# Kernel tuning notes

Measured on AMD Instinct MI355X. Metric: run time of the kernel, lower is better.

## Reference

```python
import jax, jax.numpy as jnp
import numpy as np

KS = 4          # kernel_size per pseudo-dim (open linear B-splines, degree 1)
GRID = 28       # level-0 grid side
BATCH = 256     # number of graphs
NUM_FIRST_FC = 49


def _grid(n, B):
    """Batched 8-neighborhood grid graph with 2D pseudo-coords in [0,1]."""
    rs, cs = np.meshgrid(np.arange(n), np.arange(n), indexing='ij')
    idx = rs * n + cs
    src_l, dst_l, ps_l = [], [], []
    for dr in (-1, 0, 1):
        for dc in (-1, 0, 1):
            if dr == 0 and dc == 0:
                continue
            r2, c2 = rs + dr, cs + dc
            ok = (r2 >= 0) & (r2 < n) & (c2 >= 0) & (c2 < n)
            src_l.append(idx[ok])
            dst_l.append((r2 * n + c2)[ok])
            m = int(ok.sum())
            ps_l.append(np.stack([np.full(m, (dr + 1) / 2.0),
                                  np.full(m, (dc + 1) / 2.0)], 1))
    src = np.concatenate(src_l)
    dst = np.concatenate(dst_l)
    pseudo = np.concatenate(ps_l).astype(np.float32)
    off = (np.arange(B) * n * n)[:, None]
    src_b = (src[None] + off).reshape(-1)
    dst_b = (dst[None] + off).reshape(-1)
    return (np.stack([src_b, dst_b]).astype(np.int32),
            np.tile(pseudo, (B, 1)))


def _cluster(n, B):
    """Factor-4 (2x2 block) graclus-style cluster assignment, batched."""
    rs, cs = np.meshgrid(np.arange(n), np.arange(n), indexing='ij')
    c = ((rs // 2) * (n // 2) + (cs // 2)).reshape(-1)
    off = (np.arange(B) * (n // 2) ** 2)[:, None]
    return (c[None] + off).reshape(-1).astype(np.int32)


def setup_inputs() -> dict:
    key = jax.random.key(0)
    ks = jax.random.split(key, 16)
    e0, p0 = _grid(GRID, BATCH)          # 28x28 level
    e1, p1 = _grid(GRID // 2, BATCH)     # 14x14 level
    c0 = _cluster(GRID, BATCH)           # 784 -> 196 per graph
    c1 = _cluster(GRID // 2, BATCH)      # 196 -> 49 per graph
    N0 = BATCH * GRID * GRID
    s = 0.1
    inp = {
        'x': jax.random.normal(ks[0], (N0, 1), jnp.float32),
        'edge_index0': jnp.asarray(e0), 'pseudo0': jnp.asarray(p0),
        'edge_index1': jnp.asarray(e1), 'pseudo1': jnp.asarray(p1),
        'cluster0': jnp.asarray(c0), 'cluster1': jnp.asarray(c1),
        'W1': s * jax.random.normal(ks[1], (16, 1, 32), jnp.float32),
        'root1': s * jax.random.normal(ks[2], (1, 32), jnp.float32),
        'b1': jnp.zeros((32,), jnp.float32),
        'W2': s * jax.random.normal(ks[3], (16, 32, 32), jnp.float32),
        'root2': s * jax.random.normal(ks[4], (32, 32), jnp.float32),
        'b2': jnp.zeros((32,), jnp.float32),
        'W3': s * jax.random.normal(ks[5], (16, 32, 64), jnp.float32),
        'root3': s * jax.random.normal(ks[6], (32, 64), jnp.float32),
        'b3': jnp.zeros((64,), jnp.float32),
        'W4': s * jax.random.normal(ks[7], (16, 64, 64), jnp.float32),
        'root4': s * jax.random.normal(ks[8], (64, 64), jnp.float32),
        'b4': jnp.zeros((64,), jnp.float32),
        'fc1_W': s * jax.random.normal(ks[9], (NUM_FIRST_FC * 64, 512), jnp.float32),
        'fc1_b': jnp.zeros((512,), jnp.float32),
        'fc2_W': s * jax.random.normal(ks[10], (512, 10), jnp.float32),
        'fc2_b': jnp.zeros((10,), jnp.float32),
    }
    return inp


def spline_conv(x, src, dst, pseudo, W, root, bias):
    """SplineGCN layer: degree-1 open B-spline weighting over 2D pseudo-coords,
    mean aggregation over incoming edges, plus root weight and bias."""
    n = x.shape[0]
    pos = pseudo * (KS - 1)                       # [E,2] in [0, KS-1]
    i0f = jnp.clip(jnp.floor(pos), 0, KS - 2)
    frac = pos - i0f                              # [E,2]
    i0 = i0f.astype(jnp.int32)
    XW = jnp.einsum('ni,kio->kno', x, W)          # [K, N, out]: per-kernel transform
    msg = jnp.zeros((src.shape[0], W.shape[2]), x.dtype)
    for a in (0, 1):
        wa = frac[:, 0] if a else 1.0 - frac[:, 0]
        for b in (0, 1):
            wb = frac[:, 1] if b else 1.0 - frac[:, 1]
            k = (i0[:, 0] + a) * KS + (i0[:, 1] + b)     # flat kernel index [E]
            msg = msg + (wa * wb)[:, None] * XW[k, src]  # gather per-edge
    agg = jax.ops.segment_sum(msg, dst, num_segments=n)
    deg = jax.ops.segment_sum(jnp.ones_like(dst, dtype=x.dtype), dst,
                              num_segments=n)
    return agg / jnp.maximum(deg, 1.0)[:, None] + x @ root + bias


def pool4(x, cluster):
    # GraclusMaxPool(2): two halving levels == factor-4 cluster max-pool
    return jax.ops.segment_max(x, cluster, num_segments=x.shape[0] // 4)


def reference(x, edge_index0, pseudo0, edge_index1, pseudo1, cluster0, cluster1,
              W1, root1, b1, W2, root2, b2, W3, root3, b3, W4, root4, b4,
              fc1_W, fc1_b, fc2_W, fc2_b):
    s0, d0 = edge_index0[0], edge_index0[1]
    s1, d1 = edge_index1[0], edge_index1[1]
    h = jax.nn.elu(spline_conv(x, s0, d0, pseudo0, W1, root1, b1))
    h = jax.nn.elu(spline_conv(h, s0, d0, pseudo0, W2, root2, b2))
    h = pool4(h, cluster0)
    h = jax.nn.elu(spline_conv(h, s1, d1, pseudo1, W3, root3, b3))
    h = jax.nn.elu(spline_conv(h, s1, d1, pseudo1, W4, root4, b4))
    h = pool4(h, cluster1)
    h = h.reshape(-1, NUM_FIRST_FC * 64)           # [B, 49*64]
    h = jax.nn.elu(h @ fc1_W + fc1_b)
    # dropout is identity in eval / deterministic reference
    logits = h @ fc2_W + fc2_b
    return jax.nn.log_softmax(logits, axis=-1)
```

## Files before the change

kernel.cpp:

```cpp
#include <hip/hip_runtime.h>

typedef unsigned short u16;
typedef short bf16x8 __attribute__((ext_vector_type(8)));
typedef float f32x4 __attribute__((ext_vector_type(4)));

__device__ __constant__ const int DRS[8] = {-1,-1,-1, 0, 0, 1, 1, 1};
__device__ __constant__ const int DCS[8] = {-1, 0, 1,-1, 1,-1, 0, 1};

__device__ inline float bf2f(u16 u) { return __uint_as_float(((unsigned)u) << 16); }
__device__ inline u16 f2bf(float f) {
  unsigned u = __float_as_uint(f);
  return (u16)((u + 0x7fffu + ((u >> 16) & 1u)) >> 16);
}
__device__ inline float eluf(float v) { return v > 0.f ? v : (__expf(v) - 1.f); }

__device__ inline float weff_val(const float* __restrict__ W, int d, int off, int stride) {
  int dd = d >= 4 ? d + 1 : d;
  int dr = dd / 3 - 1, dc = dd - (dd / 3) * 3 - 1;
  int kr0, kr1, nr; float wr0, wr1;
  if (dr < 0)       { kr0 = 0; wr0 = 1.f; kr1 = 0; wr1 = 0.f; nr = 1; }
  else if (dr == 0) { kr0 = 1; wr0 = .5f; kr1 = 2; wr1 = .5f; nr = 2; }
  else              { kr0 = 3; wr0 = 1.f; kr1 = 0; wr1 = 0.f; nr = 1; }
  int kc0, kc1, nc; float wc0, wc1;
  if (dc < 0)       { kc0 = 0; wc0 = 1.f; kc1 = 0; wc1 = 0.f; nc = 1; }
  else if (dc == 0) { kc0 = 1; wc0 = .5f; kc1 = 2; wc1 = .5f; nc = 2; }
  else              { kc0 = 3; wc0 = 1.f; kc1 = 0; wc1 = 0.f; nc = 1; }
  float acc = wr0 * wc0 * W[(kr0 * 4 + kc0) * stride + off];
  if (nc == 2) acc += wr0 * wc1 * W[(kr0 * 4 + kc1) * stride + off];
  if (nr == 2) {
    acc += wr1 * wc0 * W[(kr1 * 4 + kc0) * stride + off];
    if (nc == 2) acc += wr1 * wc1 * W[(kr1 * 4 + kc1) * stride + off];
  }
  return acc;
}

__global__ __launch_bounds__(256) void pack_all(
    const float* __restrict__ W1,
    const float* __restrict__ W2, const float* __restrict__ rt2,
    const float* __restrict__ W3, const float* __restrict__ rt3,
    const float* __restrict__ W4, const float* __restrict__ rt4,
    const float* __restrict__ fcW,
    float* __restrict__ wf1, u16* __restrict__ wp2,
    u16* __restrict__ wp3, u16* __restrict__ wp4, u16* __restrict__ wfc) {
  int idx = blockIdx.x * 256 + threadIdx.x;
  if (idx < 256) {
    int d = idx >> 5, o = idx & 31;
    wf1[idx] = weff_val(W1, d, o, 32);
    return;
  }
  if (idx < 9472) {
    int local = idx - 256;
    int j = local & 7, l = (local >> 3) & 63, chunk = local >> 9;
    int ct = chunk & 1, tap = chunk >> 1;
    int k = (l >> 4) * 8 + j, n = ct * 16 + (l & 15);
    float v = tap < 8 ? weff_val(W2, tap, k * 32 + n, 1024) : rt2[k * 32 + n];
    wp2[local] = f2bf(v);
    return;
  }
  if (idx < 27904) {
    int local = idx - 9472;
    int j = local & 7, l = (local >> 3) & 63, chunk = local >> 9;
    int ct = chunk & 3, tap = chunk >> 2;
    int k = (l >> 4) * 8 + j, n = ct * 16 + (l & 15);
    float v = tap < 8 ? weff_val(W3, tap, k * 64 + n, 2048) : rt3[k * 64 + n];
    wp3[local] = f2bf(v);
    return;
  }
  if (idx < 64768) {
    int local = idx - 27904;
    int j = local & 7, l = (local >> 3) & 63, chunk = local >> 9;
    int q = chunk & 1, tmp = chunk >> 1;
    int ct = tmp & 3, tap = tmp >> 2;
    int k = q * 32 + (l >> 4) * 8 + j, n = ct * 16 + (l & 15);
    float v = tap < 8 ? weff_val(W4, tap, k * 64 + n, 4096) : rt4[k * 64 + n];
    wp4[local] = f2bf(v);
    return;
  }
  {
    int local = idx - 64768;
    int j = local & 7, l = (local >> 3) & 63, qnt = local >> 9;
    int q = qnt >> 5, nt = qnt & 31;
    int k = q * 32 + (l >> 4) * 8 + j;
    int n = nt * 16 + (l & 15);
    wfc[local] = f2bf(fcW[(size_t)k * 512 + n]);
  }
}

__global__ __launch_bounds__(512) void conv_mega(
    const float* __restrict__ x,
    const float* __restrict__ wf1, const float* __restrict__ rt1, const float* __restrict__ b1,
    const u16* __restrict__ wp2, const float* __restrict__ b2,
    const u16* __restrict__ wp3, const float* __restrict__ b3,
    const u16* __restrict__ wp4, const float* __restrict__ b4,
    u16* __restrict__ A6) {
  extern __shared__ char smem[];
  int4* H1 = (int4*)smem;
  int4* H3 = (int4*)smem;
  u16*  H5 = (u16*)(smem + 17408);
  float* XT = (float*)(smem + 61568);
  int4* H2 = (int4*)(smem + 61568);
  u16*  H2u = (u16*)(smem + 61568);
  int4* H4 = (int4*)(smem + 61568);
  u16*  H4u = (u16*)(smem + 61568);

  int img = blockIdx.x, tid = threadIdx.x;
  int lane = tid & 63, wid = tid >> 6;
  int kcb = lane >> 4, n0 = lane & 15;
  int4 z4 = make_int4(0, 0, 0, 0);

  bf16x8 w2[9][2];
#pragma unroll
  for (int tap = 0; tap < 9; ++tap)
#pragma unroll
    for (int cc = 0; cc < 2; ++cc)
      w2[tap][cc] = *(const bf16x8*)(wp2 + (tap * 2 + cc) * 512 + lane * 8);

  for (int i = tid; i < 3848; i += 512) H1[i] = z4;
  for (int i = tid; i < 960; i += 512) XT[i] = 0.f;
  __syncthreads();
  for (int i = tid; i < 784; i += 512) {
    int r = i / 28, c = i - 28 * (i / 28);
    XT[(r + 1) * 32 + c + 1] = x[(size_t)img * 784 + i];
  }
  __syncthreads();

  for (int px = tid; px < 784; px += 512) {
    int r = px / 28, c = px - 28 * (px / 28);
    float acc[32];
#pragma unroll
    for (int o = 0; o < 32; ++o) acc[o] = 0.f;
#pragma unroll
    for (int d = 0; d < 8; ++d) {
      float xv = XT[(r + 1 - DRS[d]) * 32 + (c + 1 - DCS[d])];
#pragma unroll
      for (int o = 0; o < 32; ++o) acc[o] = fmaf(xv, wf1[d * 32 + o], acc[o]);
    }
    float inv = 1.f / (float)((3 - (r == 0) - (r == 27)) * (3 - (c == 0) - (c == 27)) - 1);
    float xc = XT[(r + 1) * 32 + c + 1];
    unsigned pk[16];
#pragma unroll
    for (int h = 0; h < 16; ++h) {
      float v0 = eluf(acc[2 * h] * inv + xc * rt1[2 * h] + b1[2 * h]);
      float v1 = eluf(acc[2 * h + 1] * inv + xc * rt1[2 * h + 1] + b1[2 * h + 1]);
      pk[h] = (unsigned)f2bf(v0) | ((unsigned)f2bf(v1) << 16);
    }
#pragma unroll
    for (int kc = 0; kc < 4; ++kc)
      H1[kc * 962 + (r + 1) * 32 + (c + 1)] =
          make_int4(pk[4 * kc], pk[4 * kc + 1], pk[4 * kc + 2], pk[4 * kc + 3]);
  }
  __syncthreads();

  for (int t = wid; t < 49; t += 8) {
    int pxm = t * 16 + n0;
    int r = pxm / 28, c = pxm - 28 * (pxm / 28);
    f32x4 an0 = {0,0,0,0}, an1 = {0,0,0,0}, ar0 = {0,0,0,0}, ar1 = {0,0,0,0};
#pragma unroll
    for (int d = 0; d < 8; ++d) {
      bf16x8 a = *(const bf16x8*)&H1[kcb * 962 + (r + 1 - DRS[d]) * 32 + (c + 1 - DCS[d])];
      an0 = __builtin_amdgcn_mfma_f32_16x16x32_bf16(a, w2[d][0], an0, 0, 0, 0);
      an1 = __builtin_amdgcn_mfma_f32_16x16x32_bf16(a, w2[d][1], an1, 0, 0, 0);
    }
    {
      bf16x8 a = *(const bf16x8*)&H1[kcb * 962 + (r + 1) * 32 + (c + 1)];
      ar0 = __builtin_amdgcn_mfma_f32_16x16x32_bf16(a, w2[8][0], ar0, 0, 0, 0);
      ar1 = __builtin_amdgcn_mfma_f32_16x16x32_bf16(a, w2[8][1], ar1, 0, 0, 0);
    }
#pragma unroll
    for (int j = 0; j < 4; ++j) {
      int pm = t * 16 + (lane >> 4) * 4 + j;
      int rm = pm / 28, cm = pm - 28 * (pm / 28);
      float inv = 1.f / (float)((3 - (rm == 0) - (rm == 27)) * (3 - (cm == 0) - (cm == 27)) - 1);
      H2u[pm * 32 + n0]      = f2bf(eluf(an0[j] * inv + ar0[j] + b2[n0]));
      H2u[pm * 32 + 16 + n0] = f2bf(eluf(an1[j] * inv + ar1[j] + b2[16 + n0]));
    }
  }
  __syncthreads();

  for (int i = tid; i < 1032; i += 512) {
    int kc = i / 258, rem = i - 258 * kc;
    int4 v = z4;
    if (rem < 256) {
      int pr = rem >> 4, pc = rem & 15;
      if (pr >= 1 && pr <= 14 && pc >= 1 && pc <= 14) {
        int px0 = (2 * (pr - 1)) * 28 + 2 * (pc - 1);
        union { int4 q; u16 s[8]; } A, B, C, D, R;
        A.q = H2[px0 * 4 + kc]; B.q = H2[(px0 + 1) * 4 + kc];
        C.q = H2[(px0 + 28) * 4 + kc]; D.q = H2[(px0 + 29) * 4 + kc];
#pragma unroll
        for (int e = 0; e < 8; ++e)
          R.s[e] = f2bf(fmaxf(fmaxf(bf2f(A.s[e]), bf2f(B.s[e])),
                              fmaxf(bf2f(C.s[e]), bf2f(D.s[e]))));
        v = R.q;
      }
    }
    H3[i] = v;
  }
  __syncthreads();

  int ctg = wid & 3, t0 = wid >> 2;
  bf16x8 w3[9];
#pragma unroll
  for (int tap = 0; tap < 9; ++tap)
    w3[tap] = *(const bf16x8*)(wp3 + (tap * 4 + ctg) * 512 + lane * 8);
  for (int i = tid; i < 2064; i += 512) H4[i] = z4;
  __syncthreads();

  for (int t = t0; t < 13; t += 2) {
    int pxm = t * 16 + n0; if (pxm > 195) pxm = 195;
    int r = pxm / 14, c = pxm - 14 * (pxm / 14);
    f32x4 an = {0,0,0,0}, ar = {0,0,0,0};
#pragma unroll
    for (int d = 0; d < 8; ++d) {
      bf16x8 a = *(const bf16x8*)&H3[kcb * 258 + (r + 1 - DRS[d]) * 16 + (c + 1 - DCS[d])];
      an = __builtin_amdgcn_mfma_f32_16x16x32_bf16(a, w3[d], an, 0, 0, 0);
    }
    {
      bf16x8 a = *(const bf16x8*)&H3[kcb * 258 + (r + 1) * 16 + (c + 1)];
      ar = __builtin_amdgcn_mfma_f32_16x16x32_bf16(a, w3[8], ar, 0, 0, 0);
    }
#pragma unroll
    for (int j = 0; j < 4; ++j) {
      int pm = t * 16 + (lane >> 4) * 4 + j;
      if (pm < 196) {
        int rm = pm / 14, cm = pm - 14 * (pm / 14);
        float inv = 1.f / (float)((3 - (rm == 0) - (rm == 13)) * (3 - (cm == 0) - (cm == 13)) - 1);
        int n = ctg * 16 + n0;
        float v = eluf(an[j] * inv + ar[j] + b3[n]);
        H4u[((n >> 3) * 258 + (rm + 1) * 16 + (cm + 1)) * 8 + (n & 7)] = f2bf(v);
      }
    }
  }
  __syncthreads();

  bf16x8 w4[9][2];
#pragma unroll
  for (int tap = 0; tap < 9; ++tap)
#pragma unroll
    for (int q = 0; q < 2; ++q)
      w4[tap][q] = *(const bf16x8*)(wp4 + ((tap * 4 + ctg) * 2 + q) * 512 + lane * 8);

  for (int t = t0; t < 13; t += 2) {
    int pxm = t * 16 + n0; if (pxm > 195) pxm = 195;
    int r = pxm / 14, c = pxm - 14 * (pxm / 14);
    f32x4 an = {0,0,0,0}, ar = {0,0,0,0};
#pragma unroll
    for (int d = 0; d < 8; ++d) {
      int rr = r + 1 - DRS[d], c2 = c + 1 - DCS[d];
#pragma unroll
      for (int q = 0; q < 2; ++q) {
        bf16x8 a = *(const bf16x8*)&H4[(q * 4 + kcb) * 258 + rr * 16 + c2];
        an = __builtin_amdgcn_mfma_f32_16x16x32_bf16(a, w4[d][q], an, 0, 0, 0);
      }
    }
    {
#pragma unroll
      for (int q = 0; q < 2; ++q) {
        bf16x8 a = *(const bf16x8*)&H4[(q * 4 + kcb) * 258 + (r + 1) * 16 + (c + 1)];
        ar = __builtin_amdgcn_mfma_f32_16x16x32_bf16(a, w4[8][q], ar, 0, 0, 0);
      }
    }
#pragma unroll
    for (int j = 0; j < 4; ++j) {
      int pm = t * 16 + (lane >> 4) * 4 + j;
      if (pm < 196) {
        int rm = pm / 14, cm = pm - 14 * (pm / 14);
        float inv = 1.f / (float)((3 - (rm == 0) - (rm == 13)) * (3 - (cm == 0) - (cm == 13)) - 1);
        int n = ctg * 16 + n0;
        H5[pm * 64 + n] = f2bf(eluf(an[j] * inv + ar[j] + b4[n]));
      }
    }
  }
  __syncthreads();

  if (tid < 392) {
    int kc = tid & 7, q = tid >> 3;
    int r2 = q / 7, c2 = q - 7 * (q / 7);
    int px0 = (2 * r2) * 14 + 2 * c2;
    union { int4 q4; u16 s[8]; } A, B, C, D, R;
    A.q4 = *(const int4*)&H5[px0 * 64 + kc * 8];
    B.q4 = *(const int4*)&H5[(px0 + 1) * 64 + kc * 8];
    C.q4 = *(const int4*)&H5[(px0 + 14) * 64 + kc * 8];
    D.q4 = *(const int4*)&H5[(px0 + 15) * 64 + kc * 8];
#pragma unroll
    for (int e = 0; e < 8; ++e)
      R.s[e] = f2bf(fmaxf(fmaxf(bf2f(A.s[e]), bf2f(B.s[e])),
                          fmaxf(bf2f(C.s[e]), bf2f(D.s[e]))));
    *(int4*)(A6 + ((size_t)img * 49 + q) * 64 + kc * 8) = R.q4;
  }
}

__global__ __launch_bounds__(256) void fc1_mfma(
    const u16* __restrict__ A6, const u16* __restrict__ wfc,
    float* __restrict__ part) {
  int blk = blockIdx.x;
  int ks = blk % 7;
  int mn = blk / 7;
  int mt = mn & 3, nt = mn >> 2;
  int lane = threadIdx.x & 63, w = threadIdx.x >> 6;
  int n16 = nt * 4 + w;
  f32x4 acc[4];
#pragma unroll
  for (int m4 = 0; m4 < 4; ++m4) acc[m4] = {0.f, 0.f, 0.f, 0.f};
  int rbase = mt * 64 + (lane & 15);
  int kb = ks * 448 + (lane >> 4) * 8;
  for (int qq = 0; qq < 14; ++qq) {
    bf16x8 bfr = *(const bf16x8*)(wfc + ((size_t)((ks * 14 + qq) * 32 + n16)) * 512 + lane * 8);
#pragma unroll
    for (int m4 = 0; m4 < 4; ++m4) {
      bf16x8 a = *(const bf16x8*)(A6 + (size_t)(rbase + m4 * 16) * 3136 + kb + qq * 32);
      acc[m4] = __builtin_amdgcn_mfma_f32_16x16x32_bf16(a, bfr, acc[m4], 0, 0, 0);
    }
  }
#pragma unroll
  for (int m4 = 0; m4 < 4; ++m4)
#pragma unroll
    for (int j = 0; j < 4; ++j) {
      int row = mt * 64 + m4 * 16 + (lane >> 4) * 4 + j;
      int col = nt * 64 + w * 16 + (lane & 15);
      part[((size_t)ks * 256 + row) * 512 + col] = acc[m4][j];
    }
}

__global__ __launch_bounds__(64) void fc2_kernel(
    const float* __restrict__ part, const float* __restrict__ fc1b,
    const float* __restrict__ W, const float* __restrict__ bias,
    float* __restrict__ out) {
  int bb = blockIdx.x;
  int t = threadIdx.x;
  float acc[10];
#pragma unroll
  for (int o = 0; o < 10; ++o) acc[o] = 0.f;
  for (int k = t; k < 512; k += 64) {
    float s = fc1b[k];
#pragma unroll
    for (int ks = 0; ks < 7; ++ks) s += part[(size_t)ks * 131072 + bb * 512 + k];
    float xv = eluf(s);
#pragma unroll
    for (int o = 0; o < 10; ++o) acc[o] = fmaf(xv, W[k * 10 + o], acc[o]);
  }
#pragma unroll
  for (int o = 0; o < 10; ++o) {
    float v = acc[o];
#pragma unroll
    for (int s = 32; s >= 1; s >>= 1) v += __shfl_xor(v, s);
    acc[o] = v + bias[o];
  }
  float m = acc[0];
#pragma unroll
  for (int o = 1; o < 10; ++o) m = fmaxf(m, acc[o]);
  float sum = 0.f;
#pragma unroll
  for (int o = 0; o < 10; ++o) sum += __expf(acc[o] - m);
  float lse = m + __logf(sum);
  if (t < 10) out[bb * 10 + t] = acc[t] - lse;
}

extern "C" void kernel_launch(void* const* d_in, const int* in_sizes, int n_in,
                              void* d_out, int out_size, void* d_ws, size_t ws_size,
                              hipStream_t stream) {
  const float* x    = (const float*)d_in[0];
  const float* W1   = (const float*)d_in[7];
  const float* r1   = (const float*)d_in[8];
  const float* b1   = (const float*)d_in[9];
  const float* W2   = (const float*)d_in[10];
  const float* r2   = (const float*)d_in[11];
  const float* b2   = (const float*)d_in[12];
  const float* W3   = (const float*)d_in[13];
  const float* r3   = (const float*)d_in[14];
  const float* b3   = (const float*)d_in[15];
  const float* W4   = (const float*)d_in[16];
  const float* r4   = (const float*)d_in[17];
  const float* b4   = (const float*)d_in[18];
  const float* fc1W = (const float*)d_in[19];
  const float* fc1b = (const float*)d_in[20];
  const float* fc2W = (const float*)d_in[21];
  const float* fc2b = (const float*)d_in[22];

  char* wsb = (char*)d_ws;
  float* wf1  = (float*)(wsb + 0);
  u16*   wp2  = (u16*)(wsb + 1024);
  u16*   wp3  = (u16*)(wsb + 19456);
  u16*   wp4  = (u16*)(wsb + 56320);
  u16*   wfc  = (u16*)(wsb + 130048);
  u16*   A6   = (u16*)(wsb + 3341312);
  float* part = (float*)(wsb + 4946944);

  pack_all<<<6525, 256, 0, stream>>>(W1, W2, r2, W3, r3, W4, r4, fc1W,
                                     wf1, wp2, wp3, wp4, wfc);

  (void)hipFuncSetAttribute((const void*)conv_mega,
                            hipFuncAttributeMaxDynamicSharedMemorySize, 111744);
  conv_mega<<<256, 512, 111744, stream>>>(x, wf1, r1, b1, wp2, b2, wp3, b3,
                                          wp4, b4, A6);

  fc1_mfma<<<224, 256, 0, stream>>>(A6, wfc, part);
  fc2_kernel<<<256, 64, 0, stream>>>(part, fc1b, fc2W, fc2b, (float*)d_out);
}
```

Before: 62.14 us.

## Transpose fc weights via shared memory, double conv block threads, split fc1 K further

pack_all now packs the fc1 weights through a shared-memory tile, using coalesced float4 reads and int4 writes in place of per-element strided gathers, so the pack grid shrinks a lot. conv_mega runs with 1024 threads: conv2 is split across waves by output column half, conv3/conv4 iterate with stride 4, and the shared buffers are relaid so H4 zeroing merges with H3 construction and one barrier is removed. fc1 uses 14 K-splits instead of 7 to launch twice as many blocks, and fc2 sums 14 partial buffers. The cost is more partial-sum traffic, more register pressure at 1024 threads, and a larger LDS footprint.

```diff
diff --git a/kernel.cpp b/kernel.cpp
--- a/kernel.cpp
+++ b/kernel.cpp
@@ -42,7 +42,34 @@
     const float* __restrict__ fcW,
     float* __restrict__ wf1, u16* __restrict__ wp2,
     u16* __restrict__ wp3, u16* __restrict__ wp4, u16* __restrict__ wfc) {
-  int idx = blockIdx.x * 256 + threadIdx.x;
+  __shared__ u16 T[32 * 514];
+  int blk = blockIdx.x, t = threadIdx.x;
+  if (blk < 98) {
+    int q = blk;
+#pragma unroll
+    for (int i = 0; i < 16; ++i) {
+      int idx = i * 1024 + t * 4;
+      int k = idx >> 9, n = idx & 511;
+      float4 v = *reinterpret_cast<const float4*>(fcW + (size_t)(q * 32 + k) * 512 + n);
+      T[k * 514 + n]     = f2bf(v.x);
+      T[k * 514 + n + 1] = f2bf(v.y);
+      T[k * 514 + n + 2] = f2bf(v.z);
+      T[k * 514 + n + 3] = f2bf(v.w);
+    }
+    __syncthreads();
+#pragma unroll
+    for (int w = 0; w < 8; ++w) {
+      int g = w * 256 + t;
+      int nt = g >> 6, l = g & 63;
+      union { int4 q4; u16 s[8]; } R;
+#pragma unroll
+      for (int j = 0; j < 8; ++j)
+        R.s[j] = T[((l >> 4) * 8 + j) * 514 + nt * 16 + (l & 15)];
+      *reinterpret_cast<int4*>(wfc + ((size_t)(q * 32 + nt) * 64 + l) * 8) = R.q4;
+    }
+    return;
+  }
+  int idx = (blk - 98) * 256 + t;
   if (idx < 256) {
     int d = idx >> 5, o = idx & 31;
     wf1[idx] = weff_val(W1, d, o, 32);
@@ -74,19 +101,10 @@
     int k = q * 32 + (l >> 4) * 8 + j, n = ct * 16 + (l & 15);
     float v = tap < 8 ? weff_val(W4, tap, k * 64 + n, 4096) : rt4[k * 64 + n];
     wp4[local] = f2bf(v);
-    return;
-  }
-  {
-    int local = idx - 64768;
-    int j = local & 7, l = (local >> 3) & 63, qnt = local >> 9;
-    int q = qnt >> 5, nt = qnt & 31;
-    int k = q * 32 + (l >> 4) * 8 + j;
-    int n = nt * 16 + (l & 15);
-    wfc[local] = f2bf(fcW[(size_t)k * 512 + n]);
-  }
-}
-
-__global__ __launch_bounds__(512) void conv_mega(
+  }
+}
+
+__global__ __launch_bounds__(1024) void conv_mega(
     const float* __restrict__ x,
     const float* __restrict__ wf1, const float* __restrict__ rt1, const float* __restrict__ b1,
     const u16* __restrict__ wp2, const float* __restrict__ b2,
@@ -97,34 +115,27 @@
   int4* H1 = (int4*)smem;
   int4* H3 = (int4*)smem;
   u16*  H5 = (u16*)(smem + 17408);
+  int4* H4 = (int4*)(smem + 42496);
+  u16*  H4u = (u16*)(smem + 42496);
   float* XT = (float*)(smem + 61568);
-  int4* H2 = (int4*)(smem + 61568);
-  u16*  H2u = (u16*)(smem + 61568);
-  int4* H4 = (int4*)(smem + 61568);
-  u16*  H4u = (u16*)(smem + 61568);
+  int4* H2 = (int4*)(smem + 75520);
+  u16*  H2u = (u16*)(smem + 75520);
 
   int img = blockIdx.x, tid = threadIdx.x;
   int lane = tid & 63, wid = tid >> 6;
   int kcb = lane >> 4, n0 = lane & 15;
   int4 z4 = make_int4(0, 0, 0, 0);
 
-  bf16x8 w2[9][2];
-#pragma unroll
-  for (int tap = 0; tap < 9; ++tap)
-#pragma unroll
-    for (int cc = 0; cc < 2; ++cc)
-      w2[tap][cc] = *(const bf16x8*)(wp2 + (tap * 2 + cc) * 512 + lane * 8);
-
-  for (int i = tid; i < 3848; i += 512) H1[i] = z4;
-  for (int i = tid; i < 960; i += 512) XT[i] = 0.f;
-  __syncthreads();
-  for (int i = tid; i < 784; i += 512) {
-    int r = i / 28, c = i - 28 * (i / 28);
-    XT[(r + 1) * 32 + c + 1] = x[(size_t)img * 784 + i];
-  }
-  __syncthreads();
-
-  for (int px = tid; px < 784; px += 512) {
+  for (int i = tid; i < 3848; i += 1024) H1[i] = z4;
+  if (tid < 960) {
+    int r = tid >> 5, c = tid & 31;
+    bool in = (r >= 1) && (r <= 28) && (c >= 1) && (c <= 28);
+    XT[tid] = in ? x[(size_t)img * 784 + (r - 1) * 28 + (c - 1)] : 0.f;
+  }
+  __syncthreads();
+
+  if (tid < 784) {
+    int px = tid;
     int r = px / 28, c = px - 28 * (px / 28);
     float acc[32];
 #pragma unroll
@@ -151,33 +162,37 @@
   }
   __syncthreads();
 
-  for (int t = wid; t < 49; t += 8) {
-    int pxm = t * 16 + n0;
-    int r = pxm / 28, c = pxm - 28 * (pxm / 28);
-    f32x4 an0 = {0,0,0,0}, an1 = {0,0,0,0}, ar0 = {0,0,0,0}, ar1 = {0,0,0,0};
-#pragma unroll
-    for (int d = 0; d < 8; ++d) {
-      bf16x8 a = *(const bf16x8*)&H1[kcb * 962 + (r + 1 - DRS[d]) * 32 + (c + 1 - DCS[d])];
-      an0 = __builtin_amdgcn_mfma_f32_16x16x32_bf16(a, w2[d][0], an0, 0, 0, 0);
-      an1 = __builtin_amdgcn_mfma_f32_16x16x32_bf16(a, w2[d][1], an1, 0, 0, 0);
-    }
-    {
-      bf16x8 a = *(const bf16x8*)&H1[kcb * 962 + (r + 1) * 32 + (c + 1)];
-      ar0 = __builtin_amdgcn_mfma_f32_16x16x32_bf16(a, w2[8][0], ar0, 0, 0, 0);
-      ar1 = __builtin_amdgcn_mfma_f32_16x16x32_bf16(a, w2[8][1], ar1, 0, 0, 0);
-    }
-#pragma unroll
-    for (int j = 0; j < 4; ++j) {
-      int pm = t * 16 + (lane >> 4) * 4 + j;
-      int rm = pm / 28, cm = pm - 28 * (pm / 28);
-      float inv = 1.f / (float)((3 - (rm == 0) - (rm == 27)) * (3 - (cm == 0) - (cm == 27)) - 1);
-      H2u[pm * 32 + n0]      = f2bf(eluf(an0[j] * inv + ar0[j] + b2[n0]));
-      H2u[pm * 32 + 16 + n0] = f2bf(eluf(an1[j] * inv + ar1[j] + b2[16 + n0]));
-    }
-  }
-  __syncthreads();
-
-  for (int i = tid; i < 1032; i += 512) {
+  {
+    int ctg = wid & 1, t0 = wid >> 1;
+    bf16x8 w2[9];
+#pragma unroll
+    for (int tap = 0; tap < 9; ++tap)
+      w2[tap] = *(const bf16x8*)(wp2 + (tap * 2 + ctg) * 512 + lane * 8);
+    for (int t = t0; t < 49; t += 8) {
+      int pxm = t * 16 + n0;
+      int r = pxm / 28, c = pxm - 28 * (pxm / 28);
+      f32x4 an = {0,0,0,0}, ar = {0,0,0,0};
+#pragma unroll
+      for (int d = 0; d < 8; ++d) {
+        bf16x8 a = *(const bf16x8*)&H1[kcb * 962 + (r + 1 - DRS[d]) * 32 + (c + 1 - DCS[d])];
+        an = __builtin_amdgcn_mfma_f32_16x16x32_bf16(a, w2[d], an, 0, 0, 0);
+      }
+      {
+        bf16x8 a = *(const bf16x8*)&H1[kcb * 962 + (r + 1) * 32 + (c + 1)];
+        ar = __builtin_amdgcn_mfma_f32_16x16x32_bf16(a, w2[8], ar, 0, 0, 0);
+      }
+#pragma unroll
+      for (int j = 0; j < 4; ++j) {
+        int pm = t * 16 + (lane >> 4) * 4 + j;
+        int rm = pm / 28, cm = pm - 28 * (pm / 28);
+        float inv = 1.f / (float)((3 - (rm == 0) - (rm == 27)) * (3 - (cm == 0) - (cm == 27)) - 1);
+        H2u[pm * 32 + ctg * 16 + n0] = f2bf(eluf(an[j] * inv + ar[j] + b2[ctg * 16 + n0]));
+      }
+    }
+  }
+  __syncthreads();
+
+  for (int i = tid; i < 1032; i += 1024) {
     int kc = i / 258, rem = i - 258 * kc;
     int4 v = z4;
     if (rem < 256) {
@@ -196,78 +211,77 @@
     }
     H3[i] = v;
   }
+  for (int i = tid; i < 2064; i += 1024) H4[i] = z4;
   __syncthreads();
 
   int ctg = wid & 3, t0 = wid >> 2;
-  bf16x8 w3[9];
-#pragma unroll
-  for (int tap = 0; tap < 9; ++tap)
-    w3[tap] = *(const bf16x8*)(wp3 + (tap * 4 + ctg) * 512 + lane * 8);
-  for (int i = tid; i < 2064; i += 512) H4[i] = z4;
-  __syncthreads();
-
-  for (int t = t0; t < 13; t += 2) {
-    int pxm = t * 16 + n0; if (pxm > 195) pxm = 195;
-    int r = pxm / 14, c = pxm - 14 * (pxm / 14);
-    f32x4 an = {0,0,0,0}, ar = {0,0,0,0};
-#pragma unroll
-    for (int d = 0; d < 8; ++d) {
-      bf16x8 a = *(const bf16x8*)&H3[kcb * 258 + (r + 1 - DRS[d]) * 16 + (c + 1 - DCS[d])];
-      an = __builtin_amdgcn_mfma_f32_16x16x32_bf16(a, w3[d], an, 0, 0, 0);
-    }
-    {
-      bf16x8 a = *(const bf16x8*)&H3[kcb * 258 + (r + 1) * 16 + (c + 1)];
-      ar = __builtin_amdgcn_mfma_f32_16x16x32_bf16(a, w3[8], ar, 0, 0, 0);
-    }
-#pragma unroll
-    for (int j = 0; j < 4; ++j) {
-      int pm = t * 16 + (lane >> 4) * 4 + j;
-      if (pm < 196) {
-        int rm = pm / 14, cm = pm - 14 * (pm / 14);
-        float inv = 1.f / (float)((3 - (rm == 0) - (rm == 13)) * (3 - (cm == 0) - (cm == 13)) - 1);
-        int n = ctg * 16 + n0;
-        float v = eluf(an[j] * inv + ar[j] + b3[n]);
-        H4u[((n >> 3) * 258 + (rm + 1) * 16 + (cm + 1)) * 8 + (n & 7)] = f2bf(v);
-      }
-    }
-  }
-  __syncthreads();
-
-  bf16x8 w4[9][2];
-#pragma unroll
-  for (int tap = 0; tap < 9; ++tap)
-#pragma unroll
-    for (int q = 0; q < 2; ++q)
-      w4[tap][q] = *(const bf16x8*)(wp4 + ((tap * 4 + ctg) * 2 + q) * 512 + lane * 8);
-
-  for (int t = t0; t < 13; t += 2) {
-    int pxm = t * 16 + n0; if (pxm > 195) pxm = 195;
-    int r = pxm / 14, c = pxm - 14 * (pxm / 14);
-    f32x4 an = {0,0,0,0}, ar = {0,0,0,0};
-#pragma unroll
-    for (int d = 0; d < 8; ++d) {
-      int rr = r + 1 - DRS[d], c2 = c + 1 - DCS[d];
-#pragma unroll
-      for (int q = 0; q < 2; ++q) {
-        bf16x8 a = *(const bf16x8*)&H4[(q * 4 + kcb) * 258 + rr * 16 + c2];
-        an = __builtin_amdgcn_mfma_f32_16x16x32_bf16(a, w4[d][q], an, 0, 0, 0);
-      }
-    }
-    {
+  {
+    bf16x8 w3[9];
+#pragma unroll
+    for (int tap = 0; tap < 9; ++tap)
+      w3[tap] = *(const bf16x8*)(wp3 + (tap * 4 + ctg) * 512 + lane * 8);
+    for (int t = t0; t < 13; t += 4) {
+      int pxm = t * 16 + n0; if (pxm > 195) pxm = 195;
+      int r = pxm / 14, c = pxm - 14 * (pxm / 14);
+      f32x4 an = {0,0,0,0}, ar = {0,0,0,0};
+#pragma unroll
+      for (int d = 0; d < 8; ++d) {
+        bf16x8 a = *(const bf16x8*)&H3[kcb * 258 + (r + 1 - DRS[d]) * 16 + (c + 1 - DCS[d])];
+        an = __builtin_amdgcn_mfma_f32_16x16x32_bf16(a, w3[d], an, 0, 0, 0);
+      }
+      {
+        bf16x8 a = *(const bf16x8*)&H3[kcb * 258 + (r + 1) * 16 + (c + 1)];
+        ar = __builtin_amdgcn_mfma_f32_16x16x32_bf16(a, w3[8], ar, 0, 0, 0);
+      }
+#pragma unroll
+      for (int j = 0; j < 4; ++j) {
+        int pm = t * 16 + (lane >> 4) * 4 + j;
+        if (pm < 196) {
+          int rm = pm / 14, cm = pm - 14 * (pm / 14);
+          float inv = 1.f / (float)((3 - (rm == 0) - (rm == 13)) * (3 - (cm == 0) - (cm == 13)) - 1);
+          int n = ctg * 16 + n0;
+          float v = eluf(an[j] * inv + ar[j] + b3[n]);
+          H4u[((n >> 3) * 258 + (rm + 1) * 16 + (cm + 1)) * 8 + (n & 7)] = f2bf(v);
+        }
+      }
+    }
+  }
+  __syncthreads();
+
+  {
+    bf16x8 w4[9][2];
+#pragma unroll
+    for (int tap = 0; tap < 9; ++tap)
+#pragma unroll
+      for (int q = 0; q < 2; ++q)
+        w4[tap][q] = *(const bf16x8*)(wp4 + ((tap * 4 + ctg) * 2 + q) * 512 + lane * 8);
+    for (int t = t0; t < 13; t += 4) {
+      int pxm = t * 16 + n0; if (pxm > 195) pxm = 195;
+      int r = pxm / 14, c = pxm - 14 * (pxm / 14);
+      f32x4 an = {0,0,0,0}, ar = {0,0,0,0};
+#pragma unroll
+      for (int d = 0; d < 8; ++d) {
+        int rr = r + 1 - DRS[d], c2 = c + 1 - DCS[d];
+#pragma unroll
+        for (int q = 0; q < 2; ++q) {
+          bf16x8 a = *(const bf16x8*)&H4[(q * 4 + kcb) * 258 + rr * 16 + c2];
+          an = __builtin_amdgcn_mfma_f32_16x16x32_bf16(a, w4[d][q], an, 0, 0, 0);
+        }
+      }
 #pragma unroll
       for (int q = 0; q < 2; ++q) {
         bf16x8 a = *(const bf16x8*)&H4[(q * 4 + kcb) * 258 + (r + 1) * 16 + (c + 1)];
         ar = __builtin_amdgcn_mfma_f32_16x16x32_bf16(a, w4[8][q], ar, 0, 0, 0);
       }
-    }
-#pragma unroll
-    for (int j = 0; j < 4; ++j) {
-      int pm = t * 16 + (lane >> 4) * 4 + j;
-      if (pm < 196) {
-        int rm = pm / 14, cm = pm - 14 * (pm / 14);
-        float inv = 1.f / (float)((3 - (rm == 0) - (rm == 13)) * (3 - (cm == 0) - (cm == 13)) - 1);
-        int n = ctg * 16 + n0;
-        H5[pm * 64 + n] = f2bf(eluf(an[j] * inv + ar[j] + b4[n]));
+#pragma unroll
+      for (int j = 0; j < 4; ++j) {
+        int pm = t * 16 + (lane >> 4) * 4 + j;
+        if (pm < 196) {
+          int rm = pm / 14, cm = pm - 14 * (pm / 14);
+          float inv = 1.f / (float)((3 - (rm == 0) - (rm == 13)) * (3 - (cm == 0) - (cm == 13)) - 1);
+          int n = ctg * 16 + n0;
+          H5[pm * 64 + n] = f2bf(eluf(an[j] * inv + ar[j] + b4[n]));
+        }
       }
     }
   }
@@ -294,18 +308,19 @@
     const u16* __restrict__ A6, const u16* __restrict__ wfc,
     float* __restrict__ part) {
   int blk = blockIdx.x;
-  int ks = blk % 7;
-  int mn = blk / 7;
-  int mt = mn & 3, nt = mn >> 2;
+  int ks = blk >> 5;
+  int rem = blk & 31;
+  int mt = rem & 3, nt4 = rem >> 2;
   int lane = threadIdx.x & 63, w = threadIdx.x >> 6;
-  int n16 = nt * 4 + w;
+  int NT = nt4 * 4 + w;
   f32x4 acc[4];
 #pragma unroll
   for (int m4 = 0; m4 < 4; ++m4) acc[m4] = {0.f, 0.f, 0.f, 0.f};
   int rbase = mt * 64 + (lane & 15);
-  int kb = ks * 448 + (lane >> 4) * 8;
-  for (int qq = 0; qq < 14; ++qq) {
-    bf16x8 bfr = *(const bf16x8*)(wfc + ((size_t)((ks * 14 + qq) * 32 + n16)) * 512 + lane * 8);
+  int kb = ks * 224 + (lane >> 4) * 8;
+#pragma unroll
+  for (int qq = 0; qq < 7; ++qq) {
+    bf16x8 bfr = *(const bf16x8*)(wfc + ((size_t)((ks * 7 + qq) * 32 + NT) * 64 + lane) * 8);
 #pragma unroll
     for (int m4 = 0; m4 < 4; ++m4) {
       bf16x8 a = *(const bf16x8*)(A6 + (size_t)(rbase + m4 * 16) * 3136 + kb + qq * 32);
@@ -317,7 +332,7 @@
 #pragma unroll
     for (int j = 0; j < 4; ++j) {
       int row = mt * 64 + m4 * 16 + (lane >> 4) * 4 + j;
-      int col = nt * 64 + w * 16 + (lane & 15);
+      int col = NT * 16 + (lane & 15);
       part[((size_t)ks * 256 + row) * 512 + col] = acc[m4][j];
     }
 }
@@ -334,7 +349,7 @@
   for (int k = t; k < 512; k += 64) {
     float s = fc1b[k];
 #pragma unroll
-    for (int ks = 0; ks < 7; ++ks) s += part[(size_t)ks * 131072 + bb * 512 + k];
+    for (int ks = 0; ks < 14; ++ks) s += part[(size_t)ks * 131072 + bb * 512 + k];
     float xv = eluf(s);
 #pragma unroll
     for (int o = 0; o < 10; ++o) acc[o] = fmaf(xv, W[k * 10 + o], acc[o]);
@@ -386,14 +401,14 @@
   u16*   A6   = (u16*)(wsb + 3341312);
   float* part = (float*)(wsb + 4946944);
 
-  pack_all<<<6525, 256, 0, stream>>>(W1, W2, r2, W3, r3, W4, r4, fc1W,
-                                     wf1, wp2, wp3, wp4, wfc);
+  pack_all<<<351, 256, 0, stream>>>(W1, W2, r2, W3, r3, W4, r4, fc1W,
+                                    wf1, wp2, wp3, wp4, wfc);
 
   (void)hipFuncSetAttribute((const void*)conv_mega,
-                            hipFuncAttributeMaxDynamicSharedMemorySize, 111744);
-  conv_mega<<<256, 512, 111744, stream>>>(x, wf1, r1, b1, wp2, b2, wp3, b3,
-                                          wp4, b4, A6);
-
-  fc1_mfma<<<224, 256, 0, stream>>>(A6, wfc, part);
+                            hipFuncAttributeMaxDynamicSharedMemorySize, 125696);
+  conv_mega<<<256, 1024, 125696, stream>>>(x, wf1, r1, b1, wp2, b2, wp3, b3,
+                                           wp4, b4, A6);
+
+  fc1_mfma<<<448, 256, 0, stream>>>(A6, wfc, part);
   fc2_kernel<<<256, 64, 0, stream>>>(part, fc1b, fc2W, fc2b, (float*)d_out);
 }
```

Measured after the change: 54.41 us. 1.14x faster.
